# Kernel tuning notes

Hardware: AMD Instinct MI355X
Metric: run time of the kernel (lower is better)

Reference implementation:

```python
import jax, jax.numpy as jnp
import numpy as np

S, B, I, H, E = 2048, 64, 256, 512, 256


def setup_inputs() -> dict:
    key = jax.random.key(0)
    ks = jax.random.split(key, 3)
    scale_e = 1.0 / np.sqrt(H)
    scale_x = 1.0 / np.sqrt(I + E)
    return {
        "input_seq": jax.random.normal(ks[0], (S, B, I), dtype=jnp.float32),
        "h_0": jnp.zeros((B, H), dtype=jnp.float32),
        "m_0": jnp.zeros((B, E), dtype=jnp.float32),
        "W_embed": jax.random.normal(ks[1], (E, H), dtype=jnp.float32) * scale_e,
        "b_embed": jnp.zeros((E,), dtype=jnp.float32),
        "W_ih": jax.random.normal(ks[2], (H, I + E), dtype=jnp.float32) * scale_x,
        "b_ih": jnp.zeros((H,), dtype=jnp.float32),
    }


def reference(input_seq, h_0, m_0, W_embed, b_embed, W_ih, b_ih):
    # Custom RNN cell per step t:
    #   m_t = h_prev @ W_embed.T + b_embed          (embedding of previous hidden)
    #   h_t = tanh([x_t, m_prev] @ W_ih.T + b_ih)   (uses the LAGGED m_prev)
    def step(carry, x_t):
        h_prev, m_prev = carry
        m_t = h_prev @ W_embed.T + b_embed                     # [B, E]
        combined = jnp.concatenate([x_t, m_prev], axis=1)      # [B, I+E]
        h_t = jnp.tanh(combined @ W_ih.T + b_ih)               # [B, H]
        return (h_t, m_t), h_t

    (h_T, m_T), outputs = jax.lax.scan(step, (h_0, m_0), input_seq)
    return outputs, h_T, m_T
```

## Files before the change

kernel.cpp:

```cpp
#include <hip/hip_runtime.h>


#define S2    1024
#define OUT_HT 67108864
#define OUT_MT 67141632

typedef _Float16 half8 __attribute__((ext_vector_type(8)));
typedef float f32x4 __attribute__((ext_vector_type(4)));

#define OFF_W2F   0u
#define OFF_WXF   524288u
#define OFF_C2    786432u
#define OFF_AVE   788480u
#define OFF_AVO   919552u
#define OFF_MEMB  1050624u
#define OFF_HX    1116160u
#define OFF_CNT   1378304u

__global__ __launch_bounds__(256) void k_memb(const float* __restrict__ h0,
                                              const float* __restrict__ We,
                                              const float* __restrict__ be,
                                              float* __restrict__ memb) {
  __shared__ float hs[512];
  int b = blockIdx.x, e = threadIdx.x;
  for (int i = threadIdx.x; i < 512; i += 256) hs[i] = h0[b * 512 + i];
  __syncthreads();
  float acc = be[e];
  const float* wr = We + (size_t)e * 512;
  for (int h = 0; h < 512; ++h) acc += hs[h] * wr[h];
  memb[b * 256 + e] = acc;
}

__global__ __launch_bounds__(256) void k_prep(
    const float* __restrict__ We, const float* __restrict__ be,
    const float* __restrict__ Wih, const float* __restrict__ bih,
    const float* __restrict__ m0, const float* __restrict__ memb,
    _Float16* __restrict__ w2f, _Float16* __restrict__ wxf,
    float* __restrict__ c2, float* __restrict__ ave, float* __restrict__ avo,
    unsigned int* __restrict__ cnt) {
  int blk = blockIdx.x, tid = threadIdx.x;
  if (blk < 1024) {
    int idx = blk * 256 + tid;
    int k = idx & 511, n = idx >> 9;
    float acc = 0.f;
    for (int e = 0; e < 256; ++e)
      acc += We[e * 512 + k] * Wih[n * 512 + 256 + e];
    int ntile = n >> 4, nl = n & 15;
    int kch = k >> 5, kq = (k >> 3) & 3, ke = k & 7;
    int lane = kq * 16 + nl;
    w2f[(size_t)((ntile * 16 + kch) * 64 + lane) * 8 + ke] = (_Float16)acc;
  } else if (blk < 1536) {
    int idx = (blk - 1024) * 256 + tid;
    int k = idx & 255, n = idx >> 8;
    float v = Wih[n * 512 + k];
    int ntile = n >> 4, nl = n & 15;
    int kch = k >> 5, kq = (k >> 3) & 3, ke = k & 7;
    int lane = kq * 16 + nl;
    wxf[(size_t)((ntile * 8 + kch) * 64 + lane) * 8 + ke] = (_Float16)v;
  } else if (blk < 1538) {
    int j = (blk - 1536) * 256 + tid;
    float acc = bih[j];
    for (int e = 0; e < 256; ++e) acc += be[e] * Wih[j * 512 + 256 + e];
    c2[j] = acc;
  } else if (blk < 1666) {
    int i = blk - 1538;
    int b = i >> 1, j = (i & 1) * 256 + tid;
    float acc = bih[j];
    for (int e = 0; e < 256; ++e) acc += m0[b * 256 + e] * Wih[j * 512 + 256 + e];
    ave[b * 512 + j] = acc;
  } else if (blk < 1794) {
    int i = blk - 1666;
    int b = i >> 1, j = (i & 1) * 256 + tid;
    float acc = bih[j];
    for (int e = 0; e < 256; ++e) acc += memb[b * 256 + e] * Wih[j * 512 + 256 + e];
    avo[b * 512 + j] = acc;
  } else {
    if (tid < 64) cnt[tid] = 0u;
  }
}

__device__ inline float fast_tanh(float x) {
  float z = __expf(2.f * x);
  return 1.f - 2.f / (z + 1.f);
}

__global__ __launch_bounds__(256, 1) void k_main(
    const float* __restrict__ x,
    const _Float16* __restrict__ w2f, const _Float16* __restrict__ wxf,
    const float* __restrict__ c2, const float* __restrict__ ave,
    const float* __restrict__ avo, _Float16* __restrict__ hx,
    unsigned int* __restrict__ cnt, float* __restrict__ out) {
  __shared__ __align__(16) _Float16 ha[16 * 520];
  __shared__ __align__(16) _Float16 xl[2][16 * 264];

  const int tid = threadIdx.x;
  const int g = blockIdx.x & 7;
  const int w = blockIdx.x >> 3;
  const int wave = tid >> 6, lane = tid & 63;
  const int q = lane >> 4, nl = lane & 15;
  const int ntile = w * 4 + wave;
  const int j = (ntile << 4) + nl;

  half8 w2r[16];
#pragma unroll
  for (int kc = 0; kc < 16; ++kc)
    w2r[kc] = *(const half8*)(w2f + (size_t)((ntile * 16 + kc) * 64 + lane) * 8);
  half8 wxr[8];
#pragma unroll
  for (int kc = 0; kc < 8; ++kc)
    wxr[kc] = *(const half8*)(wxf + (size_t)((ntile * 8 + kc) * 64 + lane) * 8);

  const float c2l = c2[j];
  float av0[4];
#pragma unroll
  for (int r = 0; r < 4; ++r) {
    int m = q * 4 + r;
    av0[r] = (m < 8) ? ave[(g * 8 + m) * 512 + j] : avo[(g * 8 + (m & 7)) * 512 + j];
  }

  const int row = tid >> 4, seg = tid & 15;
  const int bb = g * 8 + (row & 7);

  {
    int t = (row >> 3);
    const float* xp = x + (size_t)(t * 64 + bb) * 256 + seg * 16;
    _Float16* dst = &xl[0][row * 264 + seg * 16];
#pragma unroll
    for (int i = 0; i < 16; ++i) dst[i] = (_Float16)xp[i];
  }
  __syncthreads();

  for (int s = 0; s < S2; ++s) {
    float xpre[16];
    if (s + 1 < S2) {
      int t = 2 * (s + 1) + (row >> 3);
      const float* xp = x + (size_t)(t * 64 + bb) * 256 + seg * 16;
#pragma unroll
      for (int i = 0; i < 4; ++i) {
        float4 v = *(const float4*)(xp + i * 4);
        xpre[i * 4 + 0] = v.x; xpre[i * 4 + 1] = v.y;
        xpre[i * 4 + 2] = v.z; xpre[i * 4 + 3] = v.w;
      }
    }

    f32x4 acc = {0.f, 0.f, 0.f, 0.f};

    if (s > 0) {
      if (tid == 0) {
        unsigned target = 8u * (unsigned)s;
        while (__hip_atomic_load(&cnt[g], __ATOMIC_RELAXED, __HIP_MEMORY_SCOPE_AGENT) < target)
          __builtin_amdgcn_s_sleep(1);
        __builtin_amdgcn_fence(__ATOMIC_ACQUIRE, "agent");
      }
      __syncthreads();
      const _Float16* src = hx + (size_t)((((s - 1) & 1) * 8 + g) * 16 + row) * 512;
      {
        _Float16* drow = &ha[row * 520];
#pragma unroll
        for (int i = 0; i < 4; ++i) {
          int idx = seg + 16 * i;
          *(float4*)(drow + idx * 8) = *(const float4*)(src + idx * 8);
        }
      }
      __syncthreads();
#pragma unroll
      for (int kc = 0; kc < 16; ++kc) {
        half8 a = *(const half8*)(&ha[nl * 520 + kc * 32 + q * 8]);
        acc = __builtin_amdgcn_mfma_f32_16x16x32_f16(a, w2r[kc], acc, 0, 0, 0);
      }
    }

#pragma unroll
    for (int kc = 0; kc < 8; ++kc) {
      half8 a = *(const half8*)(&xl[s & 1][nl * 264 + kc * 32 + q * 8]);
      acc = __builtin_amdgcn_mfma_f32_16x16x32_f16(a, wxr[kc], acc, 0, 0, 0);
    }

#pragma unroll
    for (int r = 0; r < 4; ++r) {
      int m = q * 4 + r;
      float pre = acc[r] + (s == 0 ? av0[r] : c2l);
      float h = fast_tanh(pre);
      int t = 2 * s + (m >> 3);
      int b = g * 8 + (m & 7);
      out[(size_t)(t * 64 + b) * 512 + j] = h;
      if (s == S2 - 1 && m >= 8) out[(size_t)OUT_HT + b * 512 + j] = h;
      hx[(size_t)(((s & 1) * 8 + g) * 16 + m) * 512 + j] = (_Float16)h;
    }

    if (s + 1 < S2) {
      _Float16* dst = &xl[(s + 1) & 1][row * 264 + seg * 16];
#pragma unroll
      for (int i = 0; i < 16; ++i) dst[i] = (_Float16)xpre[i];
    }

    __syncthreads();
    if (tid == 0)
      __hip_atomic_fetch_add(&cnt[g], 1u, __ATOMIC_RELEASE, __HIP_MEMORY_SCOPE_AGENT);
  }
}

__global__ __launch_bounds__(256) void k_mt(float* __restrict__ out,
                                            const float* __restrict__ We,
                                            const float* __restrict__ be) {
  __shared__ float hs[512];
  int b = blockIdx.x, e = threadIdx.x;
  const float* hrow = out + (size_t)(2046 * 64 + b) * 512;
  for (int i = threadIdx.x; i < 512; i += 256) hs[i] = hrow[i];
  __syncthreads();
  float acc = be[e];
  const float* wr = We + (size_t)e * 512;
  for (int h = 0; h < 512; ++h) acc += hs[h] * wr[h];
  out[(size_t)OUT_MT + b * 256 + e] = acc;
}

extern "C" void kernel_launch(void* const* d_in, const int* in_sizes, int n_in,
                              void* d_out, int out_size, void* d_ws, size_t ws_size,
                              hipStream_t stream) {
  const float* x   = (const float*)d_in[0];
  const float* h0  = (const float*)d_in[1];
  const float* m0  = (const float*)d_in[2];
  const float* We  = (const float*)d_in[3];
  const float* be  = (const float*)d_in[4];
  const float* Wih = (const float*)d_in[5];
  const float* bih = (const float*)d_in[6];
  float* out = (float*)d_out;
  char* ws = (char*)d_ws;

  _Float16* w2f = (_Float16*)(ws + OFF_W2F);
  _Float16* wxf = (_Float16*)(ws + OFF_WXF);
  float* c2   = (float*)(ws + OFF_C2);
  float* ave  = (float*)(ws + OFF_AVE);
  float* avo  = (float*)(ws + OFF_AVO);
  float* memb = (float*)(ws + OFF_MEMB);
  _Float16* hx = (_Float16*)(ws + OFF_HX);
  unsigned int* cnt = (unsigned int*)(ws + OFF_CNT);

  k_memb<<<64, 256, 0, stream>>>(h0, We, be, memb);
  k_prep<<<1795, 256, 0, stream>>>(We, be, Wih, bih, m0, memb, w2f, wxf, c2, ave, avo, cnt);
  k_main<<<64, 256, 0, stream>>>(x, w2f, wxf, c2, ave, avo, hx, cnt, out);
  k_mt<<<64, 256, 0, stream>>>(out, We, be);
}
```

Measured before the change: 4.605 ms.

## Repartition recurrent kernel into paired blocks exchanging half hidden states

The recurrent kernel shrinks from 64 blocks to 8, arranged as 4 batch groups of 16 with 2 blocks per group, each block owning half of the hidden units. Each wave now keeps four output tiles' weights in registers. Each block reuses its own half of h from shared memory and only fetches the partner block's half through global memory, synchronised by a per-pair counter with no sleep. The two 8-row batch halves are processed in alternation, which shrinks the cross-block dependency to a single partner and overlaps the local-half MFMAs with the remote load. The cost is far fewer CUs and much higher per-wave register pressure (96 half8 weight registers), plus relaxed-ordering synchronisation that relies on an explicit waitcnt.

```diff
diff --git a/kernel.cpp b/kernel.cpp
--- a/kernel.cpp
+++ b/kernel.cpp
@@ -45,17 +45,17 @@
     float acc = 0.f;
     for (int e = 0; e < 256; ++e)
       acc += We[e * 512 + k] * Wih[n * 512 + 256 + e];
-    int ntile = n >> 4, nl = n & 15;
+    int ntile = n >> 4, nlv = n & 15;
     int kch = k >> 5, kq = (k >> 3) & 3, ke = k & 7;
-    int lane = kq * 16 + nl;
+    int lane = kq * 16 + nlv;
     w2f[(size_t)((ntile * 16 + kch) * 64 + lane) * 8 + ke] = (_Float16)acc;
   } else if (blk < 1536) {
     int idx = (blk - 1024) * 256 + tid;
     int k = idx & 255, n = idx >> 8;
     float v = Wih[n * 512 + k];
-    int ntile = n >> 4, nl = n & 15;
+    int ntile = n >> 4, nlv = n & 15;
     int kch = k >> 5, kq = (k >> 3) & 3, ke = k & 7;
-    int lane = kq * 16 + nl;
+    int lane = kq * 16 + nlv;
     wxf[(size_t)((ntile * 8 + kch) * 64 + lane) * 8 + ke] = (_Float16)v;
   } else if (blk < 1538) {
     int j = (blk - 1536) * 256 + tid;
@@ -75,128 +75,170 @@
     for (int e = 0; e < 256; ++e) acc += memb[b * 256 + e] * Wih[j * 512 + 256 + e];
     avo[b * 512 + j] = acc;
   } else {
-    if (tid < 64) cnt[tid] = 0u;
-  }
-}
-
-__device__ inline float fast_tanh(float x) {
-  float z = __expf(2.f * x);
-  return 1.f - 2.f / (z + 1.f);
+    if (tid < 128)
+      __hip_atomic_store(&cnt[tid], 0u, __ATOMIC_RELAXED, __HIP_MEMORY_SCOPE_AGENT);
+  }
 }
 
 __global__ __launch_bounds__(256, 1) void k_main(
     const float* __restrict__ x,
     const _Float16* __restrict__ w2f, const _Float16* __restrict__ wxf,
     const float* __restrict__ c2, const float* __restrict__ ave,
-    const float* __restrict__ avo, _Float16* __restrict__ hx,
+    const float* __restrict__ avo, unsigned int* __restrict__ hx,
     unsigned int* __restrict__ cnt, float* __restrict__ out) {
-  __shared__ __align__(16) _Float16 ha[16 * 520];
-  __shared__ __align__(16) _Float16 xl[2][16 * 264];
+  __shared__ __align__(16) _Float16 xs[32 * 260];
+  __shared__ __align__(16) _Float16 hloc[2][16 * 260];
+  __shared__ __align__(16) _Float16 hrem[2][16 * 260];
 
   const int tid = threadIdx.x;
-  const int g = blockIdx.x & 7;
-  const int w = blockIdx.x >> 3;
-  const int wave = tid >> 6, lane = tid & 63;
+  const int g = blockIdx.x >> 1;
+  const int w = blockIdx.x & 1;
+  const int lane = tid & 63;
+  const int wave = tid >> 6;
   const int q = lane >> 4, nl = lane & 15;
-  const int ntile = w * 4 + wave;
-  const int j = (ntile << 4) + nl;
-
-  half8 w2r[16];
-#pragma unroll
-  for (int kc = 0; kc < 16; ++kc)
-    w2r[kc] = *(const half8*)(w2f + (size_t)((ntile * 16 + kc) * 64 + lane) * 8);
-  half8 wxr[8];
-#pragma unroll
-  for (int kc = 0; kc < 8; ++kc)
-    wxr[kc] = *(const half8*)(wxf + (size_t)((ntile * 8 + kc) * 64 + lane) * 8);
-
-  const float c2l = c2[j];
-  float av0[4];
-#pragma unroll
-  for (int r = 0; r < 4; ++r) {
-    int m = q * 4 + r;
-    av0[r] = (m < 8) ? ave[(g * 8 + m) * 512 + j] : avo[(g * 8 + (m & 7)) * 512 + j];
-  }
-
-  const int row = tid >> 4, seg = tid & 15;
-  const int bb = g * 8 + (row & 7);
+  const int nt0 = w * 16 + wave * 4;
+
+  half8 w2a[4][16];
+  half8 wxr[4][8];
+#pragma unroll
+  for (int i = 0; i < 4; ++i) {
+    int ntile = nt0 + i;
+#pragma unroll
+    for (int kc = 0; kc < 8; ++kc) {
+      int kg_l = w * 8 + kc, kg_r = (1 - w) * 8 + kc;
+      w2a[i][kc]     = *(const half8*)(w2f + (size_t)((ntile * 16 + kg_l) * 64 + lane) * 8);
+      w2a[i][8 + kc] = *(const half8*)(w2f + (size_t)((ntile * 16 + kg_r) * 64 + lane) * 8);
+      wxr[i][kc]     = *(const half8*)(wxf + (size_t)((ntile * 8 + kc) * 64 + lane) * 8);
+    }
+  }
+  float c2l[4];
+#pragma unroll
+  for (int i = 0; i < 4; ++i) c2l[i] = c2[(nt0 + i) * 16 + nl];
+
+  const int r8 = tid >> 3, seg8 = tid & 7;
+  const int xb = g * 16 + (r8 & 15);
 
   {
-    int t = (row >> 3);
-    const float* xp = x + (size_t)(t * 64 + bb) * 256 + seg * 16;
-    _Float16* dst = &xl[0][row * 264 + seg * 16];
-#pragma unroll
-    for (int i = 0; i < 16; ++i) dst[i] = (_Float16)xp[i];
+    const float* xp = x + ((size_t)((r8 >> 4) * 64 + xb)) * 256 + seg8 * 32;
+#pragma unroll
+    for (int i = 0; i < 8; ++i) {
+      float4 v = *(const float4*)(xp + i * 4);
+      union { _Float16 h[4]; short4 sv; } u;
+      u.h[0] = (_Float16)v.x; u.h[1] = (_Float16)v.y;
+      u.h[2] = (_Float16)v.z; u.h[3] = (_Float16)v.w;
+      *(short4*)(&xs[r8 * 260 + seg8 * 32 + i * 4]) = u.sv;
+    }
   }
   __syncthreads();
 
+  float4 xv[8];
   for (int s = 0; s < S2; ++s) {
-    float xpre[16];
+#pragma unroll
+    for (int hf = 0; hf < 2; ++hf) {
+      if (hf == 1 && s + 1 < S2) {
+        const float* xp = x + ((size_t)((2 * s + 2 + (r8 >> 4)) * 64 + xb)) * 256 + seg8 * 32;
+#pragma unroll
+        for (int i = 0; i < 8; ++i) xv[i] = *(const float4*)(xp + i * 4);
+      }
+      _Float16* hl = hloc[hf];
+      _Float16* hr = hrem[hf];
+      unsigned int* cp = cnt + (g * 2 + hf) * 16;
+      f32x4 acc[4];
+#pragma unroll
+      for (int i = 0; i < 4; ++i) acc[i] = (f32x4){0.f, 0.f, 0.f, 0.f};
+
+      if (s > 0) {
+        unsigned int target = 8u * (unsigned int)s;
+        while (__hip_atomic_load(cp, __ATOMIC_RELAXED, __HIP_MEMORY_SCOPE_AGENT) < target) {}
+        const unsigned int* src =
+            hx + (size_t)((((((s - 1) & 1) * 4 + g) * 2 + hf) * 2 + (1 - w)) * 2048);
+        unsigned int rv[8];
+#pragma unroll
+        for (int k = 0; k < 8; ++k)
+          rv[k] = __hip_atomic_load(src + tid + k * 256, __ATOMIC_RELAXED,
+                                    __HIP_MEMORY_SCOPE_AGENT);
+#pragma unroll
+        for (int kc = 0; kc < 8; ++kc) {
+          half8 a = *(const half8*)(&hl[nl * 260 + kc * 32 + q * 8]);
+#pragma unroll
+          for (int i = 0; i < 4; ++i)
+            acc[i] = __builtin_amdgcn_mfma_f32_16x16x32_f16(a, w2a[i][kc], acc[i], 0, 0, 0);
+        }
+        unsigned int* dl = (unsigned int*)hr;
+#pragma unroll
+        for (int k = 0; k < 8; ++k) {
+          int d = tid + k * 256;
+          dl[(d >> 7) * 130 + (d & 127)] = rv[k];
+        }
+        __syncthreads();
+#pragma unroll
+        for (int kc = 0; kc < 8; ++kc) {
+          half8 a = *(const half8*)(&hr[nl * 260 + kc * 32 + q * 8]);
+#pragma unroll
+          for (int i = 0; i < 4; ++i)
+            acc[i] = __builtin_amdgcn_mfma_f32_16x16x32_f16(a, w2a[i][8 + kc], acc[i], 0, 0, 0);
+        }
+      } else {
+        __syncthreads();
+      }
+
+      const int xrow = (nl >> 3) * 16 + hf * 8 + (nl & 7);
+#pragma unroll
+      for (int kc = 0; kc < 8; ++kc) {
+        half8 a = *(const half8*)(&xs[xrow * 260 + kc * 32 + q * 8]);
+#pragma unroll
+        for (int i = 0; i < 4; ++i)
+          acc[i] = __builtin_amdgcn_mfma_f32_16x16x32_f16(a, wxr[i][kc], acc[i], 0, 0, 0);
+      }
+
+#pragma unroll
+      for (int i = 0; i < 4; ++i) {
+        int j = (nt0 + i) * 16 + nl;
+        int jl = j - w * 256;
+#pragma unroll
+        for (int r = 0; r < 4; ++r) {
+          int m = q * 4 + r;
+          int b = g * 16 + hf * 8 + (m & 7);
+          float base;
+          if (s == 0)
+            base = (m < 8) ? ave[(size_t)b * 512 + j] : avo[(size_t)b * 512 + j];
+          else
+            base = c2l[i];
+          float pre = acc[i][r] + base;
+          float z = __expf(2.f * pre);
+          float h = 1.f - 2.f / (z + 1.f);
+          int t = 2 * s + (m >> 3);
+          out[(size_t)(t * 64 + b) * 512 + j] = h;
+          if (s == S2 - 1 && m >= 8) out[(size_t)OUT_HT + (size_t)b * 512 + j] = h;
+          hl[m * 260 + jl] = (_Float16)h;
+        }
+      }
+      __syncthreads();
+
+      {
+        unsigned int* dst = hx + (size_t)(((((s & 1) * 4 + g) * 2 + hf) * 2 + w) * 2048);
+        const unsigned int* sl = (const unsigned int*)hl;
+#pragma unroll
+        for (int k = 0; k < 8; ++k) {
+          int d = tid + k * 256;
+          unsigned int v = sl[(d >> 7) * 130 + (d & 127)];
+          __hip_atomic_store(dst + d, v, __ATOMIC_RELAXED, __HIP_MEMORY_SCOPE_AGENT);
+        }
+        asm volatile("s_waitcnt vmcnt(0)" ::: "memory");
+        if (lane == 0)
+          __hip_atomic_fetch_add(cp, 1u, __ATOMIC_RELAXED, __HIP_MEMORY_SCOPE_AGENT);
+      }
+    }
+
     if (s + 1 < S2) {
-      int t = 2 * (s + 1) + (row >> 3);
-      const float* xp = x + (size_t)(t * 64 + bb) * 256 + seg * 16;
-#pragma unroll
-      for (int i = 0; i < 4; ++i) {
-        float4 v = *(const float4*)(xp + i * 4);
-        xpre[i * 4 + 0] = v.x; xpre[i * 4 + 1] = v.y;
-        xpre[i * 4 + 2] = v.z; xpre[i * 4 + 3] = v.w;
-      }
-    }
-
-    f32x4 acc = {0.f, 0.f, 0.f, 0.f};
-
-    if (s > 0) {
-      if (tid == 0) {
-        unsigned target = 8u * (unsigned)s;
-        while (__hip_atomic_load(&cnt[g], __ATOMIC_RELAXED, __HIP_MEMORY_SCOPE_AGENT) < target)
-          __builtin_amdgcn_s_sleep(1);
-        __builtin_amdgcn_fence(__ATOMIC_ACQUIRE, "agent");
-      }
-      __syncthreads();
-      const _Float16* src = hx + (size_t)((((s - 1) & 1) * 8 + g) * 16 + row) * 512;
-      {
-        _Float16* drow = &ha[row * 520];
-#pragma unroll
-        for (int i = 0; i < 4; ++i) {
-          int idx = seg + 16 * i;
-          *(float4*)(drow + idx * 8) = *(const float4*)(src + idx * 8);
-        }
-      }
-      __syncthreads();
-#pragma unroll
-      for (int kc = 0; kc < 16; ++kc) {
-        half8 a = *(const half8*)(&ha[nl * 520 + kc * 32 + q * 8]);
-        acc = __builtin_amdgcn_mfma_f32_16x16x32_f16(a, w2r[kc], acc, 0, 0, 0);
-      }
-    }
-
-#pragma unroll
-    for (int kc = 0; kc < 8; ++kc) {
-      half8 a = *(const half8*)(&xl[s & 1][nl * 264 + kc * 32 + q * 8]);
-      acc = __builtin_amdgcn_mfma_f32_16x16x32_f16(a, wxr[kc], acc, 0, 0, 0);
-    }
-
-#pragma unroll
-    for (int r = 0; r < 4; ++r) {
-      int m = q * 4 + r;
-      float pre = acc[r] + (s == 0 ? av0[r] : c2l);
-      float h = fast_tanh(pre);
-      int t = 2 * s + (m >> 3);
-      int b = g * 8 + (m & 7);
-      out[(size_t)(t * 64 + b) * 512 + j] = h;
-      if (s == S2 - 1 && m >= 8) out[(size_t)OUT_HT + b * 512 + j] = h;
-      hx[(size_t)(((s & 1) * 8 + g) * 16 + m) * 512 + j] = (_Float16)h;
-    }
-
-    if (s + 1 < S2) {
-      _Float16* dst = &xl[(s + 1) & 1][row * 264 + seg * 16];
-#pragma unroll
-      for (int i = 0; i < 16; ++i) dst[i] = (_Float16)xpre[i];
-    }
-
-    __syncthreads();
-    if (tid == 0)
-      __hip_atomic_fetch_add(&cnt[g], 1u, __ATOMIC_RELEASE, __HIP_MEMORY_SCOPE_AGENT);
+#pragma unroll
+      for (int i = 0; i < 8; ++i) {
+        union { _Float16 h[4]; short4 sv; } u;
+        u.h[0] = (_Float16)xv[i].x; u.h[1] = (_Float16)xv[i].y;
+        u.h[2] = (_Float16)xv[i].z; u.h[3] = (_Float16)xv[i].w;
+        *(short4*)(&xs[r8 * 260 + seg8 * 32 + i * 4]) = u.sv;
+      }
+    }
   }
 }
 
@@ -233,11 +275,11 @@
   float* ave  = (float*)(ws + OFF_AVE);
   float* avo  = (float*)(ws + OFF_AVO);
   float* memb = (float*)(ws + OFF_MEMB);
-  _Float16* hx = (_Float16*)(ws + OFF_HX);
+  unsigned int* hx  = (unsigned int*)(ws + OFF_HX);
   unsigned int* cnt = (unsigned int*)(ws + OFF_CNT);
 
   k_memb<<<64, 256, 0, stream>>>(h0, We, be, memb);
   k_prep<<<1795, 256, 0, stream>>>(We, be, Wih, bih, m0, memb, w2f, wxf, c2, ave, avo, cnt);
-  k_main<<<64, 256, 0, stream>>>(x, w2f, wxf, c2, ave, avo, hx, cnt, out);
+  k_main<<<8, 256, 0, stream>>>(x, w2f, wxf, c2, ave, avo, hx, cnt, out);
   k_mt<<<64, 256, 0, stream>>>(out, We, be);
 }
```

New measurement: 14.85 ms. +222.5%, slower.
